# Kernel optimization log

Hardware: AMD Instinct MI355X
Metric: run time of the kernel (lower is better)

## Reference

```python
import jax, jax.numpy as jnp
import numpy as np

B, S, E, H, FFN, NQ, DEPTH = 2, 2048, 1024, 16, 4096, 4, 2
DK = E // H
LN_EPS = 1e-5


def _layernorm(t, g, b):
    m = t.mean(-1, keepdims=True)
    v = ((t - m) ** 2).mean(-1, keepdims=True)
    return (t - m) / jnp.sqrt(v + LN_EPS) * g + b


def setup_inputs() -> dict:
    key = jax.random.key(0)
    ks = jax.random.split(key, 12)
    n = lambda i, shape, sc=1.0: (jax.random.normal(ks[i], shape, jnp.float32) * sc)
    return {
        "x": n(0, (B, S, E)),
        "wq": n(1, (E, E), 0.02),
        "wk": n(2, (E, E), 0.02),
        "wv": n(3, (E, E), 0.02),
        "wo": n(4, (E, E), 0.02),
        "w1": n(5, (E, FFN), 0.02),
        "b1": jnp.zeros((FFN,), jnp.float32),
        "w2": n(6, (FFN, E), 0.02),
        "b2": jnp.zeros((E,), jnp.float32),
        "qp_attn": n(7, (NQ, DEPTH)),
        "qp_ffn": n(8, (NQ, DEPTH)),
        "ln1_g": jnp.ones((E,), jnp.float32),
        "ln1_b": jnp.zeros((E,), jnp.float32),
        "ln2_g": jnp.ones((E,), jnp.float32),
        "ln2_b": jnp.zeros((E,), jnp.float32),
    }


def reference(x, wq, wk, wv, wo, w1, b1, w2, b2, qp_attn, qp_ffn,
              ln1_g, ln1_b, ln2_g, ln2_b):
    b, s, _ = x.shape
    # --- quantum attention ---
    q = (x @ wq).reshape(b, s, H, DK)
    k = (x @ wk).reshape(b, s, H, DK)
    v = (x @ wv).reshape(b, s, H, DK)
    scores = jnp.einsum('bqhd,bkhd->bhqk', q, k) / np.sqrt(DK).astype(np.float32)
    attn = jax.nn.softmax(scores, axis=-1)
    classical = jnp.einsum('bhqk,bkhd->bqhd', attn, v)  # (b, s, H, DK)
    # depth-2 RX-only circuit on |0..0>: <Z_0> = cos(sum_d params[0, d]);
    # data-independent scalar broadcast to the first NQ channels of each head
    c_attn = jnp.cos(qp_attn[0].sum())
    mixed = classical.at[..., :NQ].add(c_attn)
    attn_out = mixed.reshape(b, s, E) @ wo
    x1 = _layernorm(x + attn_out, ln1_g, ln1_b)  # dropout is identity in eval
    # --- quantum feed-forward ---
    h = x1 @ w1 + b1  # computed in the source but never consumed by the circuit
    # depth-2 RY-only circuit: <Z_0> = cos(sum_d params[0, d]) -- also data-free
    c_ffn = jnp.cos(qp_ffn[0].sum())
    qvec = jnp.zeros((FFN,), x.dtype).at[:NQ].set(c_ffn)
    ffn_out = jax.nn.relu(qvec) @ w2 + b2  # (E,), broadcast per token
    return _layernorm(x1 + ffn_out, ln2_g, ln2_b)
```

## Files before the change

kernel.cpp:

```cpp
#include <hip/hip_runtime.h>
#include <hip/hip_bf16.h>

typedef unsigned short u16;
using short8 = __attribute__((ext_vector_type(8))) short;
using f32x4  = __attribute__((ext_vector_type(4))) float;
using u32x2  = __attribute__((ext_vector_type(2))) unsigned;

#define S_  2048
#define E_  1024
#define H_  16
#define DK_ 64

#define GLP(p)  ((const __attribute__((address_space(1))) void*)(p))
#define LDSP(p) ((__attribute__((address_space(3))) void*)(p))

__device__ __forceinline__ float b2f(u16 u) {
  union { unsigned int i; float f; } v; v.i = ((unsigned int)u) << 16; return v.f;
}
__device__ __forceinline__ u16 f2b(float f) {
  union { float f; unsigned int i; } v; v.f = f;
  unsigned int r = v.i + 0x7fffu + ((v.i >> 16) & 1u);
  return (u16)(r >> 16);
}
__device__ __forceinline__ unsigned pk2(float a, float b) {
  __hip_bfloat162 h = __float22bfloat162_rn(make_float2(a, b));
  union { __hip_bfloat162 h; unsigned u; } c; c.h = h; return c.u;
}
__device__ __forceinline__ float fexp2(float x) {
#if __has_builtin(__builtin_amdgcn_exp2f)
  return __builtin_amdgcn_exp2f(x);
#else
  return exp2f(x);
#endif
}
__device__ __forceinline__ void plane32_swap(unsigned &dst, unsigned &src) {
#if __has_builtin(__builtin_amdgcn_permlane32_swap)
  u32x2 r = __builtin_amdgcn_permlane32_swap(dst, src, false, false);
  dst = r[0]; src = r[1];
#else
  asm volatile("v_permlane32_swap_b32 %0, %1" : "+v"(dst), "+v"(src));
#endif
}
__device__ __forceinline__ void plane16_swap(unsigned &dst, unsigned &src) {
#if __has_builtin(__builtin_amdgcn_permlane16_swap)
  u32x2 r = __builtin_amdgcn_permlane16_swap(dst, src, false, false);
  dst = r[0]; src = r[1];
#else
  asm volatile("v_permlane16_swap_b32 %0, %1" : "+v"(dst), "+v"(src));
#endif
}

__global__ __launch_bounds__(256) void prep_k(
    const float* __restrict__ x,
    const float* __restrict__ wq, const float* __restrict__ wk,
    const float* __restrict__ wv, const float* __restrict__ wo,
    const float* __restrict__ w2, const float* __restrict__ b2,
    const float* __restrict__ qpf,
    u16* __restrict__ xb, u16* __restrict__ wt, float* __restrict__ fv) {
  __shared__ u16 tile[64][65];
  int id = blockIdx.x, t = threadIdx.x;
  if (id < 2048) {
    size_t i = ((size_t)id * 256 + t) * 8;
    float4 a = *(const float4*)&x[i];
    float4 b = *(const float4*)&x[i + 4];
    uint4 o;
    o.x = pk2(a.x, a.y); o.y = pk2(a.z, a.w);
    o.z = pk2(b.x, b.y); o.w = pk2(b.z, b.w);
    *(uint4*)&xb[i] = o;
  } else if (id < 3072) {
    int i = id - 2048;
    int z = i >> 8; i &= 255;
    const float* src = (z == 0) ? wq : (z == 1) ? wk : (z == 2) ? wv : wo;
    u16* dst = wt + (size_t)z * E_ * E_;
    int k0 = (i & 15) * 64, n0 = (i >> 4) * 64;
    int rr = t >> 4, c4 = (t & 15) * 4;
    for (int p = 0; p < 4; p++) {
      int r = p * 16 + rr;
      float4 v = *(const float4*)&src[(size_t)(k0 + r) * E_ + n0 + c4];
      tile[r][c4] = f2b(v.x); tile[r][c4 + 1] = f2b(v.y);
      tile[r][c4 + 2] = f2b(v.z); tile[r][c4 + 3] = f2b(v.w);
    }
    __syncthreads();
    for (int p = 0; p < 4; p++) {
      int r = p * 16 + rr;
      ushort4 o;
      o.x = tile[c4][r]; o.y = tile[c4 + 1][r]; o.z = tile[c4 + 2][r]; o.w = tile[c4 + 3][r];
      *(ushort4*)&dst[(size_t)(n0 + r) * E_ + k0 + c4] = o;
    }
  } else {
    int e = (id - 3072) * 256 + t;
    float r = fmaxf(cosf(qpf[0] + qpf[1]), 0.f);
    fv[e] = b2[e] + r * (w2[0 * E_ + e] + w2[1 * E_ + e] + w2[2 * E_ + e] + w2[3 * E_ + e]);
  }
}

__device__ __forceinline__ void gemm_loop97(
    const u16* __restrict__ A, const u16* __restrict__ Bt,
    int m0, int n0, f32x4 acc[4][4], u16 (*As)[128][32], u16 (*Bs)[128][32]) {
  int t = threadIdx.x, lane = t & 63, w = t >> 6;
  int wm = w >> 1, wn = w & 1, l15 = lane & 15, quad = lane >> 4;
  int srow = lane >> 2, sch = (lane & 3) * 8;
  const u16 *ga[2], *gb[2];
#pragma unroll
  for (int p = 0; p < 2; p++) {
    int seg = w * 2 + p;
    ga[p] = A + (size_t)(m0 + seg * 16 + srow) * E_ + sch;
    gb[p] = Bt + (size_t)(n0 + seg * 16 + srow) * E_ + sch;
  }
#pragma unroll
  for (int p = 0; p < 2; p++) {
    int seg = w * 2 + p;
    __builtin_amdgcn_global_load_lds(GLP(ga[p]), LDSP(&As[0][seg * 16][0]), 16, 0, 0);
    __builtin_amdgcn_global_load_lds(GLP(gb[p]), LDSP(&Bs[0][seg * 16][0]), 16, 0, 0);
    ga[p] += 32; gb[p] += 32;
  }
  for (int i = 0; i < 32; i++) {
    __syncthreads();
    if (i + 1 < 32) {
      int nb = (i + 1) & 1;
#pragma unroll
      for (int p = 0; p < 2; p++) {
        int seg = w * 2 + p;
        __builtin_amdgcn_global_load_lds(GLP(ga[p]), LDSP(&As[nb][seg * 16][0]), 16, 0, 0);
        __builtin_amdgcn_global_load_lds(GLP(gb[p]), LDSP(&Bs[nb][seg * 16][0]), 16, 0, 0);
        ga[p] += 32; gb[p] += 32;
      }
    }
    int cb = i & 1;
    short8 af[4], bf[4];
#pragma unroll
    for (int ii = 0; ii < 4; ii++) af[ii] = *(const short8*)&As[cb][wm * 64 + ii * 16 + l15][quad * 8];
#pragma unroll
    for (int j = 0; j < 4; j++) bf[j] = *(const short8*)&Bs[cb][wn * 64 + j * 16 + l15][quad * 8];
#pragma unroll
    for (int ii = 0; ii < 4; ii++)
#pragma unroll
      for (int j = 0; j < 4; j++)
        acc[ii][j] = __builtin_amdgcn_mfma_f32_16x16x32_bf16(af[ii], bf[j], acc[ii][j], 0, 0, 0);
  }
}

__global__ __launch_bounds__(256) void qkv_gemm(
    const u16* __restrict__ xb, const u16* __restrict__ wt,
    u16* __restrict__ q, u16* __restrict__ k, u16* __restrict__ vt) {
  __shared__ __align__(16) u16 As[2][128][32];
  __shared__ __align__(16) u16 Bs[2][128][32];
  int bid = blockIdx.x + blockIdx.y * 8;
  int swz = (bid & 7) * 32 + (bid >> 3);
  int n0 = (swz & 7) * 128, m0 = (swz >> 3) * 128, z = blockIdx.z;
  const u16* Bt = wt + (size_t)z * E_ * E_;
  f32x4 acc[4][4];
  f32x4 zero = {0.f, 0.f, 0.f, 0.f};
  for (int i = 0; i < 4; i++)
    for (int j = 0; j < 4; j++) acc[i][j] = zero;
  gemm_loop97(xb, Bt, m0, n0, acc, As, Bs);
  int t = threadIdx.x, lane = t & 63, w = t >> 6;
  int wm = w >> 1, wn = w & 1, l15 = lane & 15, quad = lane >> 4;
  if (z < 2) {
    u16* out = (z == 0) ? q : k;
    float sc = (z == 0) ? 0.18033688f : 1.f;
#pragma unroll
    for (int i = 0; i < 4; i++)
#pragma unroll
      for (int j = 0; j < 4; j++) {
        int mm = m0 + wm * 64 + i * 16 + quad * 4;
        int nn = n0 + wn * 64 + j * 16 + l15;
#pragma unroll
        for (int rr = 0; rr < 4; rr++)
          out[(size_t)(mm + rr) * E_ + nn] = f2b(acc[i][j][rr] * sc);
      }
  } else {
#pragma unroll
    for (int i = 0; i < 4; i++)
#pragma unroll
      for (int j = 0; j < 4; j++) {
        int mm = m0 + wm * 64 + i * 16 + quad * 4;
        int nn = n0 + wn * 64 + j * 16 + l15;
        int b = mm >> 11, s = mm & (S_ - 1);
        size_t base = ((size_t)(b * H_ + (nn >> 6)) * DK_ + (nn & 63)) * S_ + s;
        ushort4 pk;
        pk.x = f2b(acc[i][j][0]); pk.y = f2b(acc[i][j][1]);
        pk.z = f2b(acc[i][j][2]); pk.w = f2b(acc[i][j][3]);
        *(ushort4*)&vt[base] = pk;
      }
  }
}

__global__ __launch_bounds__(256) void oproj_gemm(
    const u16* __restrict__ am, const u16* __restrict__ wot, float* __restrict__ proj) {
  __shared__ __align__(16) u16 As[2][128][32];
  __shared__ __align__(16) u16 Bs[2][64][32];
  int bid = blockIdx.x + blockIdx.y * 16;
  int swz = (bid & 7) * 64 + (bid >> 3);
  int n0 = (swz & 15) * 64, m0 = (swz >> 4) * 128;
  int t = threadIdx.x, lane = t & 63, w = t >> 6;
  int l15 = lane & 15, quad = lane >> 4;
  int srow = lane >> 2, sch = (lane & 3) * 8;
  const u16 *ga[2], *gb;
#pragma unroll
  for (int p = 0; p < 2; p++)
    ga[p] = am + (size_t)(m0 + (w * 2 + p) * 16 + srow) * E_ + sch;
  gb = wot + (size_t)(n0 + w * 16 + srow) * E_ + sch;
#pragma unroll
  for (int p = 0; p < 2; p++) {
    __builtin_amdgcn_global_load_lds(GLP(ga[p]), LDSP(&As[0][(w * 2 + p) * 16][0]), 16, 0, 0);
    ga[p] += 32;
  }
  __builtin_amdgcn_global_load_lds(GLP(gb), LDSP(&Bs[0][w * 16][0]), 16, 0, 0);
  gb += 32;
  f32x4 acc[2][4];
  f32x4 zero = {0.f, 0.f, 0.f, 0.f};
  for (int i = 0; i < 2; i++)
    for (int j = 0; j < 4; j++) acc[i][j] = zero;
  for (int i = 0; i < 32; i++) {
    __syncthreads();
    if (i + 1 < 32) {
      int nb = (i + 1) & 1;
#pragma unroll
      for (int p = 0; p < 2; p++) {
        __builtin_amdgcn_global_load_lds(GLP(ga[p]), LDSP(&As[nb][(w * 2 + p) * 16][0]), 16, 0, 0);
        ga[p] += 32;
      }
      __builtin_amdgcn_global_load_lds(GLP(gb), LDSP(&Bs[nb][w * 16][0]), 16, 0, 0);
      gb += 32;
    }
    int cb = i & 1;
    short8 af[2], bf[4];
#pragma unroll
    for (int ii = 0; ii < 2; ii++) af[ii] = *(const short8*)&As[cb][w * 32 + ii * 16 + l15][quad * 8];
#pragma unroll
    for (int j = 0; j < 4; j++) bf[j] = *(const short8*)&Bs[cb][j * 16 + l15][quad * 8];
#pragma unroll
    for (int ii = 0; ii < 2; ii++)
#pragma unroll
      for (int j = 0; j < 4; j++)
        acc[ii][j] = __builtin_amdgcn_mfma_f32_16x16x32_bf16(af[ii], bf[j], acc[ii][j], 0, 0, 0);
  }
#pragma unroll
  for (int i = 0; i < 2; i++)
#pragma unroll
    for (int j = 0; j < 4; j++) {
      int mm = m0 + w * 32 + i * 16 + quad * 4;
      int nn = n0 + j * 16 + l15;
#pragma unroll
      for (int rr = 0; rr < 4; rr++)
        proj[(size_t)(mm + rr) * E_ + nn] = acc[i][j][rr];
    }
}

__global__ __launch_bounds__(256, 4) void attn_kernel(
    const u16* __restrict__ q, const u16* __restrict__ kk,
    const u16* __restrict__ vt, const float* __restrict__ qpa,
    u16* __restrict__ outm) {
  __shared__ __align__(16) u16 KV[2][2][64][64];
  int bid = blockIdx.x + blockIdx.y * 32;
  int swz = (bid & 7) * 128 + (bid >> 3);
  int qt = swz & 31, bh = swz >> 5;
  int b = bh >> 4, h = bh & 15;
  int q0 = qt * 64;
  int t = threadIdx.x, lane = t & 63, w = t >> 6;
  int l15 = lane & 15, quad = lane >> 4;
  int qh = w >> 1, kh = w & 1;
  float c_attn = cosf(qpa[0] + qpa[1]);
  int r8 = lane >> 3, slot = lane & 7;
  size_t kbase = (size_t)(b * S_) * E_ + h * DK_;
  size_t vbase = (size_t)(b * H_ + h) * DK_ * S_;
  const u16 *kptr[2], *vptr[2];
#pragma unroll
  for (int p = 0; p < 2; p++) {
    int row = w * 16 + p * 8 + r8;
    int c = slot ^ (row & 7);
    kptr[p] = kk + kbase + (size_t)row * E_ + c * 8;
    vptr[p] = vt + vbase + (size_t)row * S_ + c * 8;
    __builtin_amdgcn_global_load_lds(GLP(kptr[p]), LDSP(&KV[0][0][w * 16 + p * 8][0]), 16, 0, 0);
    __builtin_amdgcn_global_load_lds(GLP(vptr[p]), LDSP(&KV[0][1][w * 16 + p * 8][0]), 16, 0, 0);
    kptr[p] += (size_t)64 * E_;
    vptr[p] += 64;
  }
  short8 bq[2][2];
#pragma unroll
  for (int nb = 0; nb < 2; nb++) {
    const u16* gq = q + (size_t)(b * S_ + q0 + qh * 32 + nb * 16 + l15) * E_ + h * DK_ + quad * 8;
    bq[nb][0] = *(const short8*)gq;
    bq[nb][1] = *(const short8*)(gq + 32);
  }
  short8 bones;
#pragma unroll
  for (int i = 0; i < 8; i++) bones[i] = (short)0x3F80;
  f32x4 O[2][4], Osum[2];
  f32x4 zero = {0.f, 0.f, 0.f, 0.f};
#pragma unroll
  for (int nb = 0; nb < 2; nb++) {
    Osum[nb] = zero;
#pragma unroll
    for (int j = 0; j < 4; j++) O[nb][j] = zero;
  }
  __syncthreads();
  for (int kt = 0; kt < S_ / 64; kt++) {
    if (kt) __syncthreads();
    if (kt + 1 < S_ / 64) {
      int nb2 = (kt + 1) & 1;
#pragma unroll
      for (int p = 0; p < 2; p++) {
        __builtin_amdgcn_global_load_lds(GLP(kptr[p]), LDSP(&KV[nb2][0][w * 16 + p * 8][0]), 16, 0, 0);
        __builtin_amdgcn_global_load_lds(GLP(vptr[p]), LDSP(&KV[nb2][1][w * 16 + p * 8][0]), 16, 0, 0);
        kptr[p] += (size_t)64 * E_;
        vptr[p] += 64;
      }
    }
    int cb = kt & 1;
    f32x4 sc[2][2];
    __builtin_amdgcn_s_setprio(1);
#pragma unroll
    for (int mb = 0; mb < 2; mb++) {
      int row = kh * 32 + mb * 16 + l15;
      int c0 = quad ^ (row & 7);
      short8 a0 = *(const short8*)&KV[cb][0][row][c0 * 8];
      short8 a1 = *(const short8*)&KV[cb][0][row][(c0 ^ 4) * 8];
#pragma unroll
      for (int nb = 0; nb < 2; nb++) {
        f32x4 z = __builtin_amdgcn_mfma_f32_16x16x32_bf16(a0, bq[nb][0], zero, 0, 0, 0);
        sc[mb][nb] = __builtin_amdgcn_mfma_f32_16x16x32_bf16(a1, bq[nb][1], z, 0, 0, 0);
      }
    }
    __builtin_amdgcn_s_setprio(0);
    short8 bv[4];
#pragma unroll
    for (int nd = 0; nd < 4; nd++) {
      int rv = nd * 16 + l15;
      int cv = (quad | (kh << 2)) ^ (rv & 7);
      bv[nd] = *(const short8*)&KV[cb][1][rv][cv * 8];
    }
    unsigned W[2][2][2];
#pragma unroll
    for (int mb = 0; mb < 2; mb++)
#pragma unroll
      for (int nb = 0; nb < 2; nb++) {
        float p0 = fexp2(sc[mb][nb][0]);
        float p1 = fexp2(sc[mb][nb][1]);
        float p2 = fexp2(sc[mb][nb][2]);
        float p3 = fexp2(sc[mb][nb][3]);
        W[mb][nb][0] = pk2(p0, p1);
        W[mb][nb][1] = pk2(p2, p3);
      }
    union AP { unsigned u[4]; short8 s; };
    AP ap[2];
#pragma unroll
    for (int nb = 0; nb < 2; nb++)
#pragma unroll
      for (int hh = 0; hh < 2; hh++) {
        unsigned a = W[0][nb][hh], bw = W[1][nb][hh];
        plane32_swap(bw, a);
        plane16_swap(a, bw);
        ap[nb].u[hh] = a; ap[nb].u[2 + hh] = bw;
      }
    __builtin_amdgcn_s_setprio(1);
#pragma unroll
    for (int nb = 0; nb < 2; nb++) {
#pragma unroll
      for (int nd = 0; nd < 4; nd++)
        O[nb][nd] = __builtin_amdgcn_mfma_f32_16x16x32_bf16(ap[nb].s, bv[nd], O[nb][nd], 0, 0, 0);
      Osum[nb] = __builtin_amdgcn_mfma_f32_16x16x32_bf16(ap[nb].s, bones, Osum[nb], 0, 0, 0);
    }
    __builtin_amdgcn_s_setprio(0);
  }
  float* red = (float*)KV;
  __syncthreads();
  if (kh) {
    float* dst = red + ((size_t)(qh * 64 + lane)) * 44;
#pragma unroll
    for (int nb = 0; nb < 2; nb++) {
#pragma unroll
      for (int nd = 0; nd < 4; nd++)
        *(f32x4*)&dst[nb * 16 + nd * 4] = O[nb][nd];
      *(f32x4*)&dst[32 + nb * 4] = Osum[nb];
    }
  }
  __syncthreads();
  if (!kh) {
    const float* src = red + ((size_t)(qh * 64 + lane)) * 44;
#pragma unroll
    for (int nb = 0; nb < 2; nb++) {
#pragma unroll
      for (int nd = 0; nd < 4; nd++) {
        f32x4 o2 = *(const f32x4*)&src[nb * 16 + nd * 4];
#pragma unroll
        for (int r = 0; r < 4; r++) O[nb][nd][r] += o2[r];
      }
      f32x4 s2 = *(const f32x4*)&src[32 + nb * 4];
#pragma unroll
      for (int r = 0; r < 4; r++) Osum[nb][r] += s2[r];
    }
#pragma unroll
    for (int nb = 0; nb < 2; nb++) {
      float inv[4];
#pragma unroll
      for (int r = 0; r < 4; r++) inv[r] = 1.f / Osum[nb][r];
#pragma unroll
      for (int nd = 0; nd < 4; nd++)
#pragma unroll
        for (int r = 0; r < 4; r++) {
          float val = O[nb][nd][r] * inv[r];
          int d = nd * 16 + l15;
          if (nd == 0 && l15 < 4) val += c_attn;
          int tok = b * S_ + q0 + qh * 32 + nb * 16 + quad * 4 + r;
          outm[(size_t)tok * E_ + h * DK_ + d] = f2b(val);
        }
    }
  }
}

__global__ __launch_bounds__(256) void ln_fused(
    const float* __restrict__ x, const float* __restrict__ proj, const float* __restrict__ fv,
    const float* __restrict__ g1, const float* __restrict__ bb1,
    const float* __restrict__ g2, const float* __restrict__ bb2,
    float* __restrict__ out) {
  __shared__ float sm[8];
  int tok = blockIdx.x, t = threadIdx.x;
  int e0 = t * 4;
  float4 xv = *(const float4*)&x[(size_t)tok * E_ + e0];
  float4 pv = *(const float4*)&proj[(size_t)tok * E_ + e0];
  float v0 = xv.x + pv.x, v1 = xv.y + pv.y;
  float v2 = xv.z + pv.z, v3 = xv.w + pv.w;
  float s = v0 + v1 + v2 + v3;
  float sq = v0 * v0 + v1 * v1 + v2 * v2 + v3 * v3;
  for (int m = 32; m >= 1; m >>= 1) { s += __shfl_xor(s, m, 64); sq += __shfl_xor(sq, m, 64); }
  int wid = t >> 6, lane = t & 63;
  if (lane == 0) { sm[wid] = s; sm[4 + wid] = sq; }
  __syncthreads();
  s = sm[0] + sm[1] + sm[2] + sm[3];
  sq = sm[4] + sm[5] + sm[6] + sm[7];
  float mean = s * (1.f / E_);
  float var = sq * (1.f / E_) - mean * mean;
  float rstd = rsqrtf(var + 1e-5f);
  float4 g1v = *(const float4*)&g1[e0];
  float4 b1v = *(const float4*)&bb1[e0];
  float4 fvv = *(const float4*)&fv[e0];
  float t0 = (v0 - mean) * rstd * g1v.x + b1v.x + fvv.x;
  float t1 = (v1 - mean) * rstd * g1v.y + b1v.y + fvv.y;
  float t2 = (v2 - mean) * rstd * g1v.z + b1v.z + fvv.z;
  float t3 = (v3 - mean) * rstd * g1v.w + b1v.w + fvv.w;
  float s2 = t0 + t1 + t2 + t3;
  float sq2 = t0 * t0 + t1 * t1 + t2 * t2 + t3 * t3;
  for (int m = 32; m >= 1; m >>= 1) { s2 += __shfl_xor(s2, m, 64); sq2 += __shfl_xor(sq2, m, 64); }
  __syncthreads();
  if (lane == 0) { sm[wid] = s2; sm[4 + wid] = sq2; }
  __syncthreads();
  s2 = sm[0] + sm[1] + sm[2] + sm[3];
  sq2 = sm[4] + sm[5] + sm[6] + sm[7];
  float mean2 = s2 * (1.f / E_);
  float var2 = sq2 * (1.f / E_) - mean2 * mean2;
  float rstd2 = rsqrtf(var2 + 1e-5f);
  float4 g2v = *(const float4*)&g2[e0];
  float4 b2v = *(const float4*)&bb2[e0];
  float4 ov;
  ov.x = (t0 - mean2) * rstd2 * g2v.x + b2v.x;
  ov.y = (t1 - mean2) * rstd2 * g2v.y + b2v.y;
  ov.z = (t2 - mean2) * rstd2 * g2v.z + b2v.z;
  ov.w = (t3 - mean2) * rstd2 * g2v.w + b2v.w;
  *(float4*)&out[(size_t)tok * E_ + e0] = ov;
}

extern "C" void kernel_launch(void* const* d_in, const int* in_sizes, int n_in,
                              void* d_out, int out_size, void* d_ws, size_t ws_size,
                              hipStream_t stream) {
  const float* x   = (const float*)d_in[0];
  const float* wq  = (const float*)d_in[1];
  const float* wk  = (const float*)d_in[2];
  const float* wv  = (const float*)d_in[3];
  const float* wo  = (const float*)d_in[4];
  const float* w2  = (const float*)d_in[7];
  const float* b2  = (const float*)d_in[8];
  const float* qpa = (const float*)d_in[9];
  const float* qpf = (const float*)d_in[10];
  const float* g1  = (const float*)d_in[11];
  const float* bb1 = (const float*)d_in[12];
  const float* g2  = (const float*)d_in[13];
  const float* bb2 = (const float*)d_in[14];

  char* ws = (char*)d_ws;
  u16* wt     = (u16*)ws;
  u16* q      = (u16*)(ws + (size_t)8  * 1048576);
  u16* k      = (u16*)(ws + (size_t)16 * 1048576);
  float* proj = (float*)(ws + (size_t)8 * 1048576);
  float* fv   = (float*)(ws + (size_t)24 * 1048576);
  u16* xb     = (u16*)d_out;
  u16* am     = (u16*)d_out;
  u16* vt     = (u16*)d_out + (size_t)4 * 1048576;
  float* outp = (float*)d_out;

  prep_k<<<dim3(3076), 256, 0, stream>>>(x, wq, wk, wv, wo, w2, b2, qpf, xb, wt, fv);
  qkv_gemm<<<dim3(8, 32, 3), 256, 0, stream>>>(xb, wt, q, k, vt);
  attn_kernel<<<dim3(32, 32), 256, 0, stream>>>(q, k, vt, qpa, am);
  oproj_gemm<<<dim3(16, 32), 256, 0, stream>>>(am, wt + (size_t)3 * E_ * E_, proj);
  ln_fused<<<dim3(4096), 256, 0, stream>>>(x, proj, fv, g1, bb1, g2, bb2, outp);
}
```

Before: 235.2 us.

## Triple-buffer LDS in QKV and output-projection GEMMs with two-stage prefetch

Both GEMM main loops move from double to triple LDS buffering. Loads are issued two k-steps ahead, and __syncthreads is replaced by a partial s_waitcnt vmcnt plus an explicit s_barrier. The goal is to keep more global-to-LDS traffic in flight and hide memory latency behind MFMA work. The cost is 50% more LDS per block, and correctness now depends on the hand-written vmcnt counts matching the number of outstanding loads.

```diff
diff --git a/kernel.cpp b/kernel.cpp
--- a/kernel.cpp
+++ b/kernel.cpp
@@ -108,16 +108,22 @@
     gb[p] = Bt + (size_t)(n0 + seg * 16 + srow) * E_ + sch;
   }
 #pragma unroll
-  for (int p = 0; p < 2; p++) {
-    int seg = w * 2 + p;
-    __builtin_amdgcn_global_load_lds(GLP(ga[p]), LDSP(&As[0][seg * 16][0]), 16, 0, 0);
-    __builtin_amdgcn_global_load_lds(GLP(gb[p]), LDSP(&Bs[0][seg * 16][0]), 16, 0, 0);
-    ga[p] += 32; gb[p] += 32;
-  }
+  for (int b2 = 0; b2 < 2; b2++)
+#pragma unroll
+    for (int p = 0; p < 2; p++) {
+      int seg = w * 2 + p;
+      __builtin_amdgcn_global_load_lds(GLP(ga[p]), LDSP(&As[b2][seg * 16][0]), 16, 0, 0);
+      __builtin_amdgcn_global_load_lds(GLP(gb[p]), LDSP(&Bs[b2][seg * 16][0]), 16, 0, 0);
+      ga[p] += 32; gb[p] += 32;
+    }
+  int idx = 0;
   for (int i = 0; i < 32; i++) {
-    __syncthreads();
-    if (i + 1 < 32) {
-      int nb = (i + 1) & 1;
+    if (i < 31) asm volatile("s_waitcnt vmcnt(4)" ::: "memory");
+    else        asm volatile("s_waitcnt vmcnt(0)" ::: "memory");
+    __builtin_amdgcn_s_barrier();
+    __builtin_amdgcn_sched_barrier(0);
+    if (i + 2 < 32) {
+      int nb = idx + 2; if (nb >= 3) nb -= 3;
 #pragma unroll
       for (int p = 0; p < 2; p++) {
         int seg = w * 2 + p;
@@ -126,25 +132,25 @@
         ga[p] += 32; gb[p] += 32;
       }
     }
-    int cb = i & 1;
     short8 af[4], bf[4];
 #pragma unroll
-    for (int ii = 0; ii < 4; ii++) af[ii] = *(const short8*)&As[cb][wm * 64 + ii * 16 + l15][quad * 8];
-#pragma unroll
-    for (int j = 0; j < 4; j++) bf[j] = *(const short8*)&Bs[cb][wn * 64 + j * 16 + l15][quad * 8];
+    for (int ii = 0; ii < 4; ii++) af[ii] = *(const short8*)&As[idx][wm * 64 + ii * 16 + l15][quad * 8];
+#pragma unroll
+    for (int j = 0; j < 4; j++) bf[j] = *(const short8*)&Bs[idx][wn * 64 + j * 16 + l15][quad * 8];
 #pragma unroll
     for (int ii = 0; ii < 4; ii++)
 #pragma unroll
       for (int j = 0; j < 4; j++)
         acc[ii][j] = __builtin_amdgcn_mfma_f32_16x16x32_bf16(af[ii], bf[j], acc[ii][j], 0, 0, 0);
+    idx = (idx + 1 == 3) ? 0 : idx + 1;
   }
 }
 
 __global__ __launch_bounds__(256) void qkv_gemm(
     const u16* __restrict__ xb, const u16* __restrict__ wt,
     u16* __restrict__ q, u16* __restrict__ k, u16* __restrict__ vt) {
-  __shared__ __align__(16) u16 As[2][128][32];
-  __shared__ __align__(16) u16 Bs[2][128][32];
+  __shared__ __align__(16) u16 As[3][128][32];
+  __shared__ __align__(16) u16 Bs[3][128][32];
   int bid = blockIdx.x + blockIdx.y * 8;
   int swz = (bid & 7) * 32 + (bid >> 3);
   int n0 = (swz & 7) * 128, m0 = (swz >> 3) * 128, z = blockIdx.z;
@@ -188,8 +194,8 @@
 
 __global__ __launch_bounds__(256) void oproj_gemm(
     const u16* __restrict__ am, const u16* __restrict__ wot, float* __restrict__ proj) {
-  __shared__ __align__(16) u16 As[2][128][32];
-  __shared__ __align__(16) u16 Bs[2][64][32];
+  __shared__ __align__(16) u16 As[3][128][32];
+  __shared__ __align__(16) u16 Bs[3][64][32];
   int bid = blockIdx.x + blockIdx.y * 16;
   int swz = (bid & 7) * 64 + (bid >> 3);
   int n0 = (swz & 15) * 64, m0 = (swz >> 4) * 128;
@@ -202,20 +208,27 @@
     ga[p] = am + (size_t)(m0 + (w * 2 + p) * 16 + srow) * E_ + sch;
   gb = wot + (size_t)(n0 + w * 16 + srow) * E_ + sch;
 #pragma unroll
-  for (int p = 0; p < 2; p++) {
-    __builtin_amdgcn_global_load_lds(GLP(ga[p]), LDSP(&As[0][(w * 2 + p) * 16][0]), 16, 0, 0);
-    ga[p] += 32;
-  }
-  __builtin_amdgcn_global_load_lds(GLP(gb), LDSP(&Bs[0][w * 16][0]), 16, 0, 0);
-  gb += 32;
+  for (int b2 = 0; b2 < 2; b2++) {
+#pragma unroll
+    for (int p = 0; p < 2; p++) {
+      __builtin_amdgcn_global_load_lds(GLP(ga[p]), LDSP(&As[b2][(w * 2 + p) * 16][0]), 16, 0, 0);
+      ga[p] += 32;
+    }
+    __builtin_amdgcn_global_load_lds(GLP(gb), LDSP(&Bs[b2][w * 16][0]), 16, 0, 0);
+    gb += 32;
+  }
   f32x4 acc[2][4];
   f32x4 zero = {0.f, 0.f, 0.f, 0.f};
   for (int i = 0; i < 2; i++)
     for (int j = 0; j < 4; j++) acc[i][j] = zero;
+  int idx = 0;
   for (int i = 0; i < 32; i++) {
-    __syncthreads();
-    if (i + 1 < 32) {
-      int nb = (i + 1) & 1;
+    if (i < 31) asm volatile("s_waitcnt vmcnt(3)" ::: "memory");
+    else        asm volatile("s_waitcnt vmcnt(0)" ::: "memory");
+    __builtin_amdgcn_s_barrier();
+    __builtin_amdgcn_sched_barrier(0);
+    if (i + 2 < 32) {
+      int nb = idx + 2; if (nb >= 3) nb -= 3;
 #pragma unroll
       for (int p = 0; p < 2; p++) {
         __builtin_amdgcn_global_load_lds(GLP(ga[p]), LDSP(&As[nb][(w * 2 + p) * 16][0]), 16, 0, 0);
@@ -224,17 +237,17 @@
       __builtin_amdgcn_global_load_lds(GLP(gb), LDSP(&Bs[nb][w * 16][0]), 16, 0, 0);
       gb += 32;
     }
-    int cb = i & 1;
     short8 af[2], bf[4];
 #pragma unroll
-    for (int ii = 0; ii < 2; ii++) af[ii] = *(const short8*)&As[cb][w * 32 + ii * 16 + l15][quad * 8];
-#pragma unroll
-    for (int j = 0; j < 4; j++) bf[j] = *(const short8*)&Bs[cb][j * 16 + l15][quad * 8];
+    for (int ii = 0; ii < 2; ii++) af[ii] = *(const short8*)&As[idx][w * 32 + ii * 16 + l15][quad * 8];
+#pragma unroll
+    for (int j = 0; j < 4; j++) bf[j] = *(const short8*)&Bs[idx][j * 16 + l15][quad * 8];
 #pragma unroll
     for (int ii = 0; ii < 2; ii++)
 #pragma unroll
       for (int j = 0; j < 4; j++)
         acc[ii][j] = __builtin_amdgcn_mfma_f32_16x16x32_bf16(af[ii], bf[j], acc[ii][j], 0, 0, 0);
+    idx = (idx + 1 == 3) ? 0 : idx + 1;
   }
 #pragma unroll
   for (int i = 0; i < 2; i++)
```

Result: no change. 237.2 us, median of 2 (+0.9%).

## Retile QKV GEMM to 128x64 blocks and triple-buffer the O-projection GEMM

Applied to the files above, without the earlier changes.

The QKV GEMM moves from 128x128 tiles with four 64x64 warp tiles to the 128x64 tile layout already used by the O-projection, which doubles the grid to 16x32x3 blocks. This gives more blocks per CU and better occupancy, at the cost of more redundant reads of A. The O-projection GEMM becomes a three-stage LDS pipeline that prefetches two K-steps ahead, with explicit vmcnt waits and a raw s_barrier replacing __syncthreads. The deeper prefetch is meant to hide global-to-LDS latency better, but it uses more LDS and relies on hand-tuned waitcnt correctness.

```diff
diff --git a/kernel.cpp b/kernel.cpp
--- a/kernel.cpp
+++ b/kernel.cpp
@@ -94,113 +94,23 @@
   }
 }
 
-__device__ __forceinline__ void gemm_loop97(
-    const u16* __restrict__ A, const u16* __restrict__ Bt,
-    int m0, int n0, f32x4 acc[4][4], u16 (*As)[128][32], u16 (*Bs)[128][32]) {
-  int t = threadIdx.x, lane = t & 63, w = t >> 6;
-  int wm = w >> 1, wn = w & 1, l15 = lane & 15, quad = lane >> 4;
-  int srow = lane >> 2, sch = (lane & 3) * 8;
-  const u16 *ga[2], *gb[2];
-#pragma unroll
-  for (int p = 0; p < 2; p++) {
-    int seg = w * 2 + p;
-    ga[p] = A + (size_t)(m0 + seg * 16 + srow) * E_ + sch;
-    gb[p] = Bt + (size_t)(n0 + seg * 16 + srow) * E_ + sch;
-  }
-#pragma unroll
-  for (int p = 0; p < 2; p++) {
-    int seg = w * 2 + p;
-    __builtin_amdgcn_global_load_lds(GLP(ga[p]), LDSP(&As[0][seg * 16][0]), 16, 0, 0);
-    __builtin_amdgcn_global_load_lds(GLP(gb[p]), LDSP(&Bs[0][seg * 16][0]), 16, 0, 0);
-    ga[p] += 32; gb[p] += 32;
-  }
-  for (int i = 0; i < 32; i++) {
-    __syncthreads();
-    if (i + 1 < 32) {
-      int nb = (i + 1) & 1;
-#pragma unroll
-      for (int p = 0; p < 2; p++) {
-        int seg = w * 2 + p;
-        __builtin_amdgcn_global_load_lds(GLP(ga[p]), LDSP(&As[nb][seg * 16][0]), 16, 0, 0);
-        __builtin_amdgcn_global_load_lds(GLP(gb[p]), LDSP(&Bs[nb][seg * 16][0]), 16, 0, 0);
-        ga[p] += 32; gb[p] += 32;
-      }
-    }
-    int cb = i & 1;
-    short8 af[4], bf[4];
-#pragma unroll
-    for (int ii = 0; ii < 4; ii++) af[ii] = *(const short8*)&As[cb][wm * 64 + ii * 16 + l15][quad * 8];
-#pragma unroll
-    for (int j = 0; j < 4; j++) bf[j] = *(const short8*)&Bs[cb][wn * 64 + j * 16 + l15][quad * 8];
-#pragma unroll
-    for (int ii = 0; ii < 4; ii++)
-#pragma unroll
-      for (int j = 0; j < 4; j++)
-        acc[ii][j] = __builtin_amdgcn_mfma_f32_16x16x32_bf16(af[ii], bf[j], acc[ii][j], 0, 0, 0);
-  }
-}
-
 __global__ __launch_bounds__(256) void qkv_gemm(
     const u16* __restrict__ xb, const u16* __restrict__ wt,
     u16* __restrict__ q, u16* __restrict__ k, u16* __restrict__ vt) {
   __shared__ __align__(16) u16 As[2][128][32];
-  __shared__ __align__(16) u16 Bs[2][128][32];
-  int bid = blockIdx.x + blockIdx.y * 8;
-  int swz = (bid & 7) * 32 + (bid >> 3);
-  int n0 = (swz & 7) * 128, m0 = (swz >> 3) * 128, z = blockIdx.z;
-  const u16* Bt = wt + (size_t)z * E_ * E_;
-  f32x4 acc[4][4];
-  f32x4 zero = {0.f, 0.f, 0.f, 0.f};
-  for (int i = 0; i < 4; i++)
-    for (int j = 0; j < 4; j++) acc[i][j] = zero;
-  gemm_loop97(xb, Bt, m0, n0, acc, As, Bs);
-  int t = threadIdx.x, lane = t & 63, w = t >> 6;
-  int wm = w >> 1, wn = w & 1, l15 = lane & 15, quad = lane >> 4;
-  if (z < 2) {
-    u16* out = (z == 0) ? q : k;
-    float sc = (z == 0) ? 0.18033688f : 1.f;
-#pragma unroll
-    for (int i = 0; i < 4; i++)
-#pragma unroll
-      for (int j = 0; j < 4; j++) {
-        int mm = m0 + wm * 64 + i * 16 + quad * 4;
-        int nn = n0 + wn * 64 + j * 16 + l15;
-#pragma unroll
-        for (int rr = 0; rr < 4; rr++)
-          out[(size_t)(mm + rr) * E_ + nn] = f2b(acc[i][j][rr] * sc);
-      }
-  } else {
-#pragma unroll
-    for (int i = 0; i < 4; i++)
-#pragma unroll
-      for (int j = 0; j < 4; j++) {
-        int mm = m0 + wm * 64 + i * 16 + quad * 4;
-        int nn = n0 + wn * 64 + j * 16 + l15;
-        int b = mm >> 11, s = mm & (S_ - 1);
-        size_t base = ((size_t)(b * H_ + (nn >> 6)) * DK_ + (nn & 63)) * S_ + s;
-        ushort4 pk;
-        pk.x = f2b(acc[i][j][0]); pk.y = f2b(acc[i][j][1]);
-        pk.z = f2b(acc[i][j][2]); pk.w = f2b(acc[i][j][3]);
-        *(ushort4*)&vt[base] = pk;
-      }
-  }
-}
-
-__global__ __launch_bounds__(256) void oproj_gemm(
-    const u16* __restrict__ am, const u16* __restrict__ wot, float* __restrict__ proj) {
-  __shared__ __align__(16) u16 As[2][128][32];
   __shared__ __align__(16) u16 Bs[2][64][32];
   int bid = blockIdx.x + blockIdx.y * 16;
   int swz = (bid & 7) * 64 + (bid >> 3);
-  int n0 = (swz & 15) * 64, m0 = (swz >> 4) * 128;
+  int n0 = (swz & 15) * 64, m0 = (swz >> 4) * 128, z = blockIdx.z;
+  const u16* Bt = wt + (size_t)z * E_ * E_;
   int t = threadIdx.x, lane = t & 63, w = t >> 6;
   int l15 = lane & 15, quad = lane >> 4;
   int srow = lane >> 2, sch = (lane & 3) * 8;
   const u16 *ga[2], *gb;
 #pragma unroll
   for (int p = 0; p < 2; p++)
-    ga[p] = am + (size_t)(m0 + (w * 2 + p) * 16 + srow) * E_ + sch;
-  gb = wot + (size_t)(n0 + w * 16 + srow) * E_ + sch;
+    ga[p] = xb + (size_t)(m0 + (w * 2 + p) * 16 + srow) * E_ + sch;
+  gb = Bt + (size_t)(n0 + w * 16 + srow) * E_ + sch;
 #pragma unroll
   for (int p = 0; p < 2; p++) {
     __builtin_amdgcn_global_load_lds(GLP(ga[p]), LDSP(&As[0][(w * 2 + p) * 16][0]), 16, 0, 0);
@@ -235,6 +145,93 @@
 #pragma unroll
       for (int j = 0; j < 4; j++)
         acc[ii][j] = __builtin_amdgcn_mfma_f32_16x16x32_bf16(af[ii], bf[j], acc[ii][j], 0, 0, 0);
+  }
+  if (z < 2) {
+    u16* out = (z == 0) ? q : k;
+    float sc = (z == 0) ? 0.18033688f : 1.f;
+#pragma unroll
+    for (int i = 0; i < 2; i++)
+#pragma unroll
+      for (int j = 0; j < 4; j++) {
+        int mm = m0 + w * 32 + i * 16 + quad * 4;
+        int nn = n0 + j * 16 + l15;
+#pragma unroll
+        for (int rr = 0; rr < 4; rr++)
+          out[(size_t)(mm + rr) * E_ + nn] = f2b(acc[i][j][rr] * sc);
+      }
+  } else {
+#pragma unroll
+    for (int i = 0; i < 2; i++)
+#pragma unroll
+      for (int j = 0; j < 4; j++) {
+        int mm = m0 + w * 32 + i * 16 + quad * 4;
+        int nn = n0 + j * 16 + l15;
+        int b = mm >> 11, s = mm & (S_ - 1);
+        size_t base = ((size_t)(b * H_ + (nn >> 6)) * DK_ + (nn & 63)) * S_ + s;
+        ushort4 pk;
+        pk.x = f2b(acc[i][j][0]); pk.y = f2b(acc[i][j][1]);
+        pk.z = f2b(acc[i][j][2]); pk.w = f2b(acc[i][j][3]);
+        *(ushort4*)&vt[base] = pk;
+      }
+  }
+}
+
+__global__ __launch_bounds__(256) void oproj_gemm(
+    const u16* __restrict__ am, const u16* __restrict__ wot, float* __restrict__ proj) {
+  __shared__ __align__(16) u16 As[3][128][32];
+  __shared__ __align__(16) u16 Bs[3][64][32];
+  int bid = blockIdx.x + blockIdx.y * 16;
+  int swz = (bid & 7) * 64 + (bid >> 3);
+  int n0 = (swz & 15) * 64, m0 = (swz >> 4) * 128;
+  int t = threadIdx.x, lane = t & 63, w = t >> 6;
+  int l15 = lane & 15, quad = lane >> 4;
+  int srow = lane >> 2, sch = (lane & 3) * 8;
+  const u16 *ga[2], *gb;
+#pragma unroll
+  for (int p = 0; p < 2; p++)
+    ga[p] = am + (size_t)(m0 + (w * 2 + p) * 16 + srow) * E_ + sch;
+  gb = wot + (size_t)(n0 + w * 16 + srow) * E_ + sch;
+#pragma unroll
+  for (int b2 = 0; b2 < 2; b2++) {
+#pragma unroll
+    for (int p = 0; p < 2; p++) {
+      __builtin_amdgcn_global_load_lds(GLP(ga[p]), LDSP(&As[b2][(w * 2 + p) * 16][0]), 16, 0, 0);
+      ga[p] += 32;
+    }
+    __builtin_amdgcn_global_load_lds(GLP(gb), LDSP(&Bs[b2][w * 16][0]), 16, 0, 0);
+    gb += 32;
+  }
+  f32x4 acc[2][4];
+  f32x4 zero = {0.f, 0.f, 0.f, 0.f};
+  for (int i = 0; i < 2; i++)
+    for (int j = 0; j < 4; j++) acc[i][j] = zero;
+  int idx = 0;
+  for (int i = 0; i < 32; i++) {
+    if (i < 31) asm volatile("s_waitcnt vmcnt(3)" ::: "memory");
+    else        asm volatile("s_waitcnt vmcnt(0)" ::: "memory");
+    __builtin_amdgcn_s_barrier();
+    __builtin_amdgcn_sched_barrier(0);
+    if (i + 2 < 32) {
+      int nb = idx + 2; if (nb >= 3) nb -= 3;
+#pragma unroll
+      for (int p = 0; p < 2; p++) {
+        __builtin_amdgcn_global_load_lds(GLP(ga[p]), LDSP(&As[nb][(w * 2 + p) * 16][0]), 16, 0, 0);
+        ga[p] += 32;
+      }
+      __builtin_amdgcn_global_load_lds(GLP(gb), LDSP(&Bs[nb][w * 16][0]), 16, 0, 0);
+      gb += 32;
+    }
+    short8 af[2], bf[4];
+#pragma unroll
+    for (int ii = 0; ii < 2; ii++) af[ii] = *(const short8*)&As[idx][w * 32 + ii * 16 + l15][quad * 8];
+#pragma unroll
+    for (int j = 0; j < 4; j++) bf[j] = *(const short8*)&Bs[idx][j * 16 + l15][quad * 8];
+#pragma unroll
+    for (int ii = 0; ii < 2; ii++)
+#pragma unroll
+      for (int j = 0; j < 4; j++)
+        acc[ii][j] = __builtin_amdgcn_mfma_f32_16x16x32_bf16(af[ii], bf[j], acc[ii][j], 0, 0, 0);
+    idx = (idx + 1 == 3) ? 0 : idx + 1;
   }
 #pragma unroll
   for (int i = 0; i < 2; i++)
@@ -490,7 +487,7 @@
   float* outp = (float*)d_out;
 
   prep_k<<<dim3(3076), 256, 0, stream>>>(x, wq, wk, wv, wo, w2, b2, qpf, xb, wt, fv);
-  qkv_gemm<<<dim3(8, 32, 3), 256, 0, stream>>>(xb, wt, q, k, vt);
+  qkv_gemm<<<dim3(16, 32, 3), 256, 0, stream>>>(xb, wt, q, k, vt);
   attn_kernel<<<dim3(32, 32), 256, 0, stream>>>(q, k, vt, qpa, am);
   oproj_gemm<<<dim3(16, 32), 256, 0, stream>>>(am, wt + (size_t)3 * E_ * E_, proj);
   ln_fused<<<dim3(4096), 256, 0, stream>>>(x, proj, fv, g1, bb1, g2, bb2, outp);
```

New measurement: 242.7 us. 1.03x slower.
